# Performance work log

Measured on AMD Instinct MI355X. Metric: run time of the kernel, lower is better.

Reference implementation:

```python
import jax, jax.numpy as jnp
import numpy as np


def setup_inputs() -> dict:
    key = jax.random.key(0)
    ks = jax.random.split(key, 6)
    B, S, T, E, D = 16, 128, 128, 512, 512  # batch, enc steps, dec steps, enc units, dec units
    scale = 0.05
    return {
        "enc": jax.random.normal(ks[0], (B, S, E), dtype=jnp.float32),
        "dec": jax.random.normal(ks[1], (B, T, D), dtype=jnp.float32),
        "W1": jax.random.normal(ks[2], (E, E), dtype=jnp.float32) * scale,
        "W2": jax.random.normal(ks[3], (D, E), dtype=jnp.float32) * scale,
        "b": jax.random.normal(ks[4], (1, 1, E), dtype=jnp.float32) * scale,
        "V": jax.random.normal(ks[5], (E, 1), dtype=jnp.float32) * scale,
    }


def reference(enc, dec, W1, W2, b, V):
    # Vectorized Bahdanau additive attention (the original loops over decoder
    # timesteps with keras.backend.rnn; the steps are independent so we batch them).
    W1_hs = jnp.einsum('bse,ef->bsf', enc, W1)            # [B,S,E] (computed once, not per step)
    W2_ht = jnp.einsum('btd,de->bte', dec, W2)            # [B,T,E]
    # tanh(W1.hs + W2.ht + b): broadcast to [B,T,S,E]
    scores = jnp.tanh(W1_hs[:, None, :, :] + W2_ht[:, :, None, :] + b)
    logits = jnp.einsum('btse,e->bts', scores, V[:, 0])   # [B,T,S]
    attn_weights = jax.nn.softmax(logits, axis=-1)        # softmax over encoder steps
    context_vectors = jnp.einsum('bts,bse->bte', attn_weights, enc)  # [B,T,E]
    return (context_vectors, attn_weights)
```

## Files before the change

### kernel.cpp

```cpp
#include <hip/hip_runtime.h>
#include <hip/hip_bf16.h>
#include <cstddef>


constexpr int nBt = 16, nSq = 128, nTq = 128, nEd = 512;

typedef __attribute__((ext_vector_type(4))) float f32x4;
typedef __attribute__((ext_vector_type(8))) short s16x8;

#define PRESCALE 2.8853900817779268f
#define LOG2E 1.4426950408889634f

__device__ __forceinline__ unsigned short to_bf(float f) {
    unsigned u = __builtin_bit_cast(unsigned, f);
    return (unsigned short)((u + 0x7FFFu + ((u >> 16) & 1u)) >> 16);
}
__device__ __forceinline__ float from_bf(unsigned short h) {
    unsigned u = ((unsigned)h) << 16;
    return __builtin_bit_cast(float, u);
}

__global__ __launch_bounds__(256) void kWprep(
    const float* __restrict__ W1, const float* __restrict__ W2,
    unsigned short* __restrict__ WT)
{
    const int z = blockIdx.z;
    const float* W = z ? W2 : W1;
    __shared__ float tl[32][33];
    const int r  = threadIdx.x >> 3;
    const int c4 = (threadIdx.x & 7) * 4;
    const int kB = blockIdx.y * 32;
    const int nB = blockIdx.x * 32;
    const float4 v = *(const float4*)&W[(size_t)(kB + r) * nEd + nB + c4];
    tl[r][c4 + 0] = v.x; tl[r][c4 + 1] = v.y;
    tl[r][c4 + 2] = v.z; tl[r][c4 + 3] = v.w;
    __syncthreads();
    unsigned short hh[4], ll[4];
    #pragma unroll
    for (int i = 0; i < 4; ++i) {
        const float x = tl[c4 + i][r];
        hh[i] = to_bf(x);
        ll[i] = to_bf(x - from_bf(hh[i]));
    }
    const size_t o = ((size_t)z * nEd + nB + r) * nEd + kB + c4;
    *(ushort4*)&WT[o] = *(ushort4*)hh;
    *(ushort4*)&WT[(size_t)2 * nEd * nEd + o] = *(ushort4*)ll;
}

__global__ __launch_bounds__(256) void kMgemmB(
    const float* __restrict__ A0, const float* __restrict__ A1,
    const unsigned short* __restrict__ WT, const float* __restrict__ bias,
    float* __restrict__ C0, float* __restrict__ C1)
{
    const int z = blockIdx.z;
    const float* __restrict__ A = z ? A1 : A0;
    const unsigned short* __restrict__ Wh = WT + (size_t)z * nEd * nEd;
    const unsigned short* __restrict__ Wl = Wh + (size_t)2 * nEd * nEd;
    float* __restrict__ C = z ? C1 : C0;

    __shared__ unsigned short sAh[32][72];
    __shared__ unsigned short sAl[32][72];
    __shared__ unsigned short sBh[128][72];
    __shared__ unsigned short sBl[128][72];

    const int tid  = threadIdx.x;
    const int lane = tid & 63;
    const int wv   = tid >> 6;
    const int rowB = blockIdx.y * 32;
    const int colB = blockIdx.x * 128;

    const int ar = tid >> 3, ak = (tid & 7) * 8;
    const int br = tid >> 1, bc = (tid & 1) * 32;

    f32x4 acc[2][2] = {};
    const int l15 = lane & 15;
    const int kh  = lane >> 4;

    for (int k0 = 0; k0 < nEd; k0 += 64) {
        const float4 ga0 = *(const float4*)&A[(size_t)(rowB + ar) * nEd + k0 + ak];
        const float4 ga1 = *(const float4*)&A[(size_t)(rowB + ar) * nEd + k0 + ak + 4];
        const size_t wo = (size_t)(colB + br) * nEd + k0 + bc;
        s16x8 gh[4], gl[4];
        #pragma unroll
        for (int j = 0; j < 4; ++j) {
            gh[j] = *(const s16x8*)&Wh[wo + 8 * j];
            gl[j] = *(const s16x8*)&Wl[wo + 8 * j];
        }

        __syncthreads();
        {
            const float a8[8] = {ga0.x, ga0.y, ga0.z, ga0.w,
                                 ga1.x, ga1.y, ga1.z, ga1.w};
            unsigned short h[8], l[8];
            #pragma unroll
            for (int i = 0; i < 8; ++i) {
                h[i] = to_bf(a8[i]);
                l[i] = to_bf(a8[i] - from_bf(h[i]));
            }
            *(ushort4*)&sAh[ar][ak]     = *(ushort4*)&h[0];
            *(ushort4*)&sAh[ar][ak + 4] = *(ushort4*)&h[4];
            *(ushort4*)&sAl[ar][ak]     = *(ushort4*)&l[0];
            *(ushort4*)&sAl[ar][ak + 4] = *(ushort4*)&l[4];
        }
        #pragma unroll
        for (int j = 0; j < 4; ++j) {
            *(s16x8*)&sBh[br][bc + 8 * j] = gh[j];
            *(s16x8*)&sBl[br][bc + 8 * j] = gl[j];
        }
        __syncthreads();

        #pragma unroll
        for (int kk = 0; kk < 2; ++kk) {
            s16x8 fAh[2], fAl[2], fBh[2], fBl[2];
            #pragma unroll
            for (int mi = 0; mi < 2; ++mi) {
                fAh[mi] = *(const s16x8*)&sAh[mi * 16 + l15][kk * 32 + kh * 8];
                fAl[mi] = *(const s16x8*)&sAl[mi * 16 + l15][kk * 32 + kh * 8];
            }
            #pragma unroll
            for (int ni = 0; ni < 2; ++ni) {
                fBh[ni] = *(const s16x8*)&sBh[wv * 32 + ni * 16 + l15][kk * 32 + kh * 8];
                fBl[ni] = *(const s16x8*)&sBl[wv * 32 + ni * 16 + l15][kk * 32 + kh * 8];
            }
            #pragma unroll
            for (int mi = 0; mi < 2; ++mi)
                #pragma unroll
                for (int ni = 0; ni < 2; ++ni) {
                    f32x4 a = acc[mi][ni];
                    a = __builtin_amdgcn_mfma_f32_16x16x32_bf16(fAh[mi], fBh[ni], a, 0, 0, 0);
                    a = __builtin_amdgcn_mfma_f32_16x16x32_bf16(fAl[mi], fBh[ni], a, 0, 0, 0);
                    a = __builtin_amdgcn_mfma_f32_16x16x32_bf16(fAh[mi], fBl[ni], a, 0, 0, 0);
                    acc[mi][ni] = a;
                }
        }
    }

    #pragma unroll
    for (int ni = 0; ni < 2; ++ni) {
        const int col = colB + wv * 32 + ni * 16 + l15;
        const float bval = z ? bias[col] : 0.0f;
        #pragma unroll
        for (int mi = 0; mi < 2; ++mi) {
            #pragma unroll
            for (int r = 0; r < 4; ++r) {
                const int row = rowB + mi * 16 + kh * 4 + r;
                C[(size_t)row * nEd + col] =
                    __builtin_amdgcn_exp2f((acc[mi][ni][r] + bval) * PRESCALE);
            }
        }
    }
}

__global__ __launch_bounds__(256) void kLogits(
    const float* __restrict__ X1e,
    const float* __restrict__ X2e,
    const float* __restrict__ V,
    float* __restrict__ lg)
{
    const int sg = blockIdx.x, tg = blockIdx.y, b = blockIdx.z;
    const int tid  = threadIdx.x;
    const int lane = tid & 63;
    const int w    = tid >> 6;
    const int s0 = sg * 32 + w * 8;
    const int t0 = tg * 8;

    const float4* vp = (const float4*)V;
    const float4  v0 = vp[lane * 2], v1 = vp[lane * 2 + 1];
    const float4 n0 = make_float4(-2.f * v0.x, -2.f * v0.y, -2.f * v0.z, -2.f * v0.w);
    const float4 n1 = make_float4(-2.f * v1.x, -2.f * v1.y, -2.f * v1.z, -2.f * v1.w);

    float4 c0[8], c1[8];
    #pragma unroll
    for (int i = 0; i < 8; ++i) {
        const float4* xp = (const float4*)(X2e + ((size_t)b * nTq + t0 + i) * nEd);
        c0[i] = xp[lane * 2];
        c1[i] = xp[lane * 2 + 1];
    }

    for (int si = 0; si < 8; ++si) {
        const int s = s0 + si;
        const float4* ap = (const float4*)(X1e + ((size_t)b * nSq + s) * nEd);
        const float4 x0 = ap[lane * 2], x1 = ap[lane * 2 + 1];
        float acc[8];
        #pragma unroll
        for (int t = 0; t < 8; ++t) {
            float a;
            a  = n0.x * __builtin_amdgcn_rcpf(fmaf(x0.x, c0[t].x, 1.0f));
            a += n0.y * __builtin_amdgcn_rcpf(fmaf(x0.y, c0[t].y, 1.0f));
            a += n0.z * __builtin_amdgcn_rcpf(fmaf(x0.z, c0[t].z, 1.0f));
            a += n0.w * __builtin_amdgcn_rcpf(fmaf(x0.w, c0[t].w, 1.0f));
            a += n1.x * __builtin_amdgcn_rcpf(fmaf(x1.x, c1[t].x, 1.0f));
            a += n1.y * __builtin_amdgcn_rcpf(fmaf(x1.y, c1[t].y, 1.0f));
            a += n1.z * __builtin_amdgcn_rcpf(fmaf(x1.z, c1[t].z, 1.0f));
            a += n1.w * __builtin_amdgcn_rcpf(fmaf(x1.w, c1[t].w, 1.0f));
            acc[t] = a;
        }
        #pragma unroll
        for (int t = 0; t < 8; ++t) {
            float a = acc[t];
            #pragma unroll
            for (int off = 32; off >= 1; off >>= 1)
                a += __shfl_xor(a, off);
            if (lane == 0)
                lg[((size_t)b * nTq + t0 + t) * nSq + s] = a;
        }
    }
}

__global__ __launch_bounds__(256) void kEncT(
    const float* __restrict__ enc, unsigned short* __restrict__ encT)
{
    const int b = blockIdx.z;
    __shared__ float tl[32][33];
    const int r  = threadIdx.x >> 3;
    const int c4 = (threadIdx.x & 7) * 4;
    const int sB = blockIdx.y * 32;
    const int eB = blockIdx.x * 32;
    const float4 v = *(const float4*)&enc[((size_t)b * nSq + sB + r) * nEd + eB + c4];
    tl[r][c4 + 0] = v.x; tl[r][c4 + 1] = v.y;
    tl[r][c4 + 2] = v.z; tl[r][c4 + 3] = v.w;
    __syncthreads();
    unsigned short o[4];
    #pragma unroll
    for (int i = 0; i < 4; ++i) o[i] = to_bf(tl[c4 + i][r]);
    *(ushort4*)&encT[((size_t)b * nEd + eB + r) * nSq + sB + c4] = *(ushort4*)o;
}

__global__ __launch_bounds__(256) void kSoft(
    float* __restrict__ attnw,
    unsigned short* __restrict__ attnbf)
{
    const int bt = blockIdx.x * 4 + (threadIdx.x >> 6);
    const int lane = threadIdx.x & 63;
    const float l0 = attnw[(size_t)bt * nSq + lane];
    const float l1 = attnw[(size_t)bt * nSq + lane + 64];
    float m = fmaxf(l0, l1);
    #pragma unroll
    for (int off = 32; off >= 1; off >>= 1)
        m = fmaxf(m, __shfl_xor(m, off));
    const float e0 = __builtin_amdgcn_exp2f((l0 - m) * LOG2E);
    const float e1 = __builtin_amdgcn_exp2f((l1 - m) * LOG2E);
    float sum = e0 + e1;
    #pragma unroll
    for (int off = 32; off >= 1; off >>= 1)
        sum += __shfl_xor(sum, off);
    const float inv = __builtin_amdgcn_rcpf(sum);
    const float w0 = e0 * inv, w1 = e1 * inv;
    attnw[(size_t)bt * nSq + lane]      = w0;
    attnw[(size_t)bt * nSq + lane + 64] = w1;
    attnbf[(size_t)bt * nSq + lane]      = to_bf(w0);
    attnbf[(size_t)bt * nSq + lane + 64] = to_bf(w1);
}

__global__ __launch_bounds__(256) void kCtxMM(
    const unsigned short* __restrict__ attnbf,
    const unsigned short* __restrict__ encT,
    float* __restrict__ ctx)
{
    const int b  = blockIdx.z;
    const int tB = blockIdx.y * 32;
    const int eB = blockIdx.x * 64;

    __shared__ unsigned short sA[32][136];
    __shared__ unsigned short sB[64][136];

    const int tid  = threadIdx.x;
    const int lane = tid & 63;
    const int w    = tid >> 6;
    const int wm = (w >> 1) * 16;
    const int wn = (w & 1) * 32;
    const int l15 = lane & 15;
    const int kh  = lane >> 4;

    {
        const int r = tid >> 3, c = (tid & 7) * 16;
        const size_t o = ((size_t)b * nTq + tB + r) * nSq + c;
        *(s16x8*)&sA[r][c]     = *(const s16x8*)&attnbf[o];
        *(s16x8*)&sA[r][c + 8] = *(const s16x8*)&attnbf[o + 8];
    }
    {
        const int r = tid >> 2, c = (tid & 3) * 32;
        const size_t o = ((size_t)b * nEd + eB + r) * nSq + c;
        *(s16x8*)&sB[r][c]      = *(const s16x8*)&encT[o];
        *(s16x8*)&sB[r][c + 8]  = *(const s16x8*)&encT[o + 8];
        *(s16x8*)&sB[r][c + 16] = *(const s16x8*)&encT[o + 16];
        *(s16x8*)&sB[r][c + 24] = *(const s16x8*)&encT[o + 24];
    }
    __syncthreads();

    f32x4 acc[2] = {};
    #pragma unroll
    for (int kk = 0; kk < 4; ++kk) {
        const s16x8 fA = *(const s16x8*)&sA[wm + l15][kk * 32 + kh * 8];
        #pragma unroll
        for (int ni = 0; ni < 2; ++ni) {
            const s16x8 fB = *(const s16x8*)&sB[wn + ni * 16 + l15][kk * 32 + kh * 8];
            acc[ni] = __builtin_amdgcn_mfma_f32_16x16x32_bf16(fA, fB, acc[ni], 0, 0, 0);
        }
    }

    #pragma unroll
    for (int ni = 0; ni < 2; ++ni) {
        const int e = eB + wn + ni * 16 + l15;
        #pragma unroll
        for (int r = 0; r < 4; ++r) {
            const int t = tB + wm + kh * 4 + r;
            ctx[((size_t)b * nTq + t) * nEd + e] = acc[ni][r];
        }
    }
}

extern "C" void kernel_launch(void* const* d_in, const int* in_sizes, int n_in,
                              void* d_out, int out_size, void* d_ws, size_t ws_size,
                              hipStream_t stream) {
    const float* enc = (const float*)d_in[0];
    const float* dec = (const float*)d_in[1];
    const float* W1  = (const float*)d_in[2];
    const float* W2  = (const float*)d_in[3];
    const float* bv  = (const float*)d_in[4];
    const float* V   = (const float*)d_in[5];

    float* ctx   = (float*)d_out;
    float* attnw = (float*)d_out + (size_t)nBt * nTq * nEd;

    unsigned short* WT = (unsigned short*)d_out;

    float* ws0 = (float*)d_ws;
    float* ws1 = ws0 + (size_t)nBt * nSq * nEd;
    unsigned short* encT   = (unsigned short*)d_ws;
    unsigned short* attnbf = (unsigned short*)((char*)d_ws + 2*1024*1024);

    kWprep<<<dim3(nEd / 32, nEd / 32, 2), dim3(256), 0, stream>>>(W1, W2, WT);
    kMgemmB<<<dim3(nEd / 128, (nBt * nSq) / 32, 2), dim3(256), 0, stream>>>(
        enc, dec, WT, bv, ws0, ws1);
    kLogits<<<dim3(4, 16, nBt), dim3(256), 0, stream>>>(ws0, ws1, V, attnw);
    kEncT<<<dim3(nEd / 32, nSq / 32, nBt), dim3(256), 0, stream>>>(enc, encT);
    kSoft<<<dim3((nBt * nTq) / 4), dim3(256), 0, stream>>>(attnw, attnbf);
    kCtxMM<<<dim3(nEd / 64, nTq / 32, nBt), dim3(256), 0, stream>>>(
        attnbf, encT, ctx);
}
```

Baseline: 60.99 us.

## Halve logits t-tile, fold V-sum constant, convert attention to bf16 inside ctx GEMM

The logits kernel now processes 4 decoder steps per block instead of 8 and launches twice as many blocks, so each thread holds fewer registers and more waves can be resident. The per-element tanh identity is rearranged so the constant sum of V is added once rather than folded into the fma form. The softmax kernel no longer writes a separate bf16 copy of the weights. Instead, the context GEMM reads the fp32 weights and converts them to bf16 while staging them into shared memory. This removes one buffer write but makes the GEMM load twice the bytes for its A operand.

```diff
diff --git a/kernel.cpp b/kernel.cpp
--- a/kernel.cpp
+++ b/kernel.cpp
@@ -162,16 +162,17 @@
     const int lane = tid & 63;
     const int w    = tid >> 6;
     const int s0 = sg * 32 + w * 8;
-    const int t0 = tg * 8;
+    const int t0 = tg * 4;
 
     const float4* vp = (const float4*)V;
     const float4  v0 = vp[lane * 2], v1 = vp[lane * 2 + 1];
     const float4 n0 = make_float4(-2.f * v0.x, -2.f * v0.y, -2.f * v0.z, -2.f * v0.w);
     const float4 n1 = make_float4(-2.f * v1.x, -2.f * v1.y, -2.f * v1.z, -2.f * v1.w);
-
-    float4 c0[8], c1[8];
-    #pragma unroll
-    for (int i = 0; i < 8; ++i) {
+    const float vsum = v0.x + v0.y + v0.z + v0.w + v1.x + v1.y + v1.z + v1.w;
+
+    float4 c0[4], c1[4];
+    #pragma unroll
+    for (int i = 0; i < 4; ++i) {
         const float4* xp = (const float4*)(X2e + ((size_t)b * nTq + t0 + i) * nEd);
         c0[i] = xp[lane * 2];
         c1[i] = xp[lane * 2 + 1];
@@ -181,22 +182,22 @@
         const int s = s0 + si;
         const float4* ap = (const float4*)(X1e + ((size_t)b * nSq + s) * nEd);
         const float4 x0 = ap[lane * 2], x1 = ap[lane * 2 + 1];
-        float acc[8];
-        #pragma unroll
-        for (int t = 0; t < 8; ++t) {
-            float a;
-            a  = n0.x * __builtin_amdgcn_rcpf(fmaf(x0.x, c0[t].x, 1.0f));
-            a += n0.y * __builtin_amdgcn_rcpf(fmaf(x0.y, c0[t].y, 1.0f));
-            a += n0.z * __builtin_amdgcn_rcpf(fmaf(x0.z, c0[t].z, 1.0f));
-            a += n0.w * __builtin_amdgcn_rcpf(fmaf(x0.w, c0[t].w, 1.0f));
-            a += n1.x * __builtin_amdgcn_rcpf(fmaf(x1.x, c1[t].x, 1.0f));
-            a += n1.y * __builtin_amdgcn_rcpf(fmaf(x1.y, c1[t].y, 1.0f));
-            a += n1.z * __builtin_amdgcn_rcpf(fmaf(x1.z, c1[t].z, 1.0f));
-            a += n1.w * __builtin_amdgcn_rcpf(fmaf(x1.w, c1[t].w, 1.0f));
+        float acc[4];
+        #pragma unroll
+        for (int t = 0; t < 4; ++t) {
+            float a = vsum;
+            a += n0.x * __builtin_amdgcn_rcpf(x0.x * c0[t].x + 1.0f);
+            a += n0.y * __builtin_amdgcn_rcpf(x0.y * c0[t].y + 1.0f);
+            a += n0.z * __builtin_amdgcn_rcpf(x0.z * c0[t].z + 1.0f);
+            a += n0.w * __builtin_amdgcn_rcpf(x0.w * c0[t].w + 1.0f);
+            a += n1.x * __builtin_amdgcn_rcpf(x1.x * c1[t].x + 1.0f);
+            a += n1.y * __builtin_amdgcn_rcpf(x1.y * c1[t].y + 1.0f);
+            a += n1.z * __builtin_amdgcn_rcpf(x1.z * c1[t].z + 1.0f);
+            a += n1.w * __builtin_amdgcn_rcpf(x1.w * c1[t].w + 1.0f);
             acc[t] = a;
         }
         #pragma unroll
-        for (int t = 0; t < 8; ++t) {
+        for (int t = 0; t < 4; ++t) {
             float a = acc[t];
             #pragma unroll
             for (int off = 32; off >= 1; off >>= 1)
@@ -226,9 +227,7 @@
     *(ushort4*)&encT[((size_t)b * nEd + eB + r) * nSq + sB + c4] = *(ushort4*)o;
 }
 
-__global__ __launch_bounds__(256) void kSoft(
-    float* __restrict__ attnw,
-    unsigned short* __restrict__ attnbf)
+__global__ __launch_bounds__(256) void kSoftW(float* __restrict__ attnw)
 {
     const int bt = blockIdx.x * 4 + (threadIdx.x >> 6);
     const int lane = threadIdx.x & 63;
@@ -245,15 +244,12 @@
     for (int off = 32; off >= 1; off >>= 1)
         sum += __shfl_xor(sum, off);
     const float inv = __builtin_amdgcn_rcpf(sum);
-    const float w0 = e0 * inv, w1 = e1 * inv;
-    attnw[(size_t)bt * nSq + lane]      = w0;
-    attnw[(size_t)bt * nSq + lane + 64] = w1;
-    attnbf[(size_t)bt * nSq + lane]      = to_bf(w0);
-    attnbf[(size_t)bt * nSq + lane + 64] = to_bf(w1);
+    attnw[(size_t)bt * nSq + lane]      = e0 * inv;
+    attnw[(size_t)bt * nSq + lane + 64] = e1 * inv;
 }
 
 __global__ __launch_bounds__(256) void kCtxMM(
-    const unsigned short* __restrict__ attnbf,
+    const float* __restrict__ attnw,
     const unsigned short* __restrict__ encT,
     float* __restrict__ ctx)
 {
@@ -274,9 +270,16 @@
 
     {
         const int r = tid >> 3, c = (tid & 7) * 16;
-        const size_t o = ((size_t)b * nTq + tB + r) * nSq + c;
-        *(s16x8*)&sA[r][c]     = *(const s16x8*)&attnbf[o];
-        *(s16x8*)&sA[r][c + 8] = *(const s16x8*)&attnbf[o + 8];
+        const float* ap = &attnw[((size_t)b * nTq + tB + r) * nSq + c];
+        unsigned short h[16];
+        #pragma unroll
+        for (int q = 0; q < 4; ++q) {
+            const float4 v = *(const float4*)(ap + 4 * q);
+            h[4 * q + 0] = to_bf(v.x); h[4 * q + 1] = to_bf(v.y);
+            h[4 * q + 2] = to_bf(v.z); h[4 * q + 3] = to_bf(v.w);
+        }
+        *(s16x8*)&sA[r][c]     = *(s16x8*)&h[0];
+        *(s16x8*)&sA[r][c + 8] = *(s16x8*)&h[8];
     }
     {
         const int r = tid >> 2, c = (tid & 3) * 32;
@@ -327,15 +330,14 @@
 
     float* ws0 = (float*)d_ws;
     float* ws1 = ws0 + (size_t)nBt * nSq * nEd;
-    unsigned short* encT   = (unsigned short*)d_ws;
-    unsigned short* attnbf = (unsigned short*)((char*)d_ws + 2*1024*1024);
+    unsigned short* encT = (unsigned short*)d_ws;
 
     kWprep<<<dim3(nEd / 32, nEd / 32, 2), dim3(256), 0, stream>>>(W1, W2, WT);
     kMgemmB<<<dim3(nEd / 128, (nBt * nSq) / 32, 2), dim3(256), 0, stream>>>(
         enc, dec, WT, bv, ws0, ws1);
-    kLogits<<<dim3(4, 16, nBt), dim3(256), 0, stream>>>(ws0, ws1, V, attnw);
+    kLogits<<<dim3(4, 32, nBt), dim3(256), 0, stream>>>(ws0, ws1, V, attnw);
     kEncT<<<dim3(nEd / 32, nSq / 32, nBt), dim3(256), 0, stream>>>(enc, encT);
-    kSoft<<<dim3((nBt * nTq) / 4), dim3(256), 0, stream>>>(attnw, attnbf);
+    kSoftW<<<dim3((nBt * nTq) / 4), dim3(256), 0, stream>>>(attnw);
     kCtxMM<<<dim3(nEd / 64, nTq / 32, nBt), dim3(256), 0, stream>>>(
-        attnbf, encT, ctx);
-}
+        attnw, encT, ctx);
+}
```

Measured after the change: 58.65 us. 3.8% less time.
